# Optimization experiments

Measured on AMD Instinct MI355X. Metric: run time of the kernel, lower is better.

## Reference

```python
import jax, jax.numpy as jnp
import numpy as np

D1, D2, B, I, O = 64, 64, 32, 64, 128


def setup_inputs() -> dict:
    key = jax.random.key(0)
    ks = jax.random.split(key, 13)
    k = float(np.sqrt(1.0 / O))
    u = lambda kk, shape: jax.random.uniform(kk, shape, minval=-k, maxval=k, dtype=jnp.float32)
    return {
        "x": jax.random.normal(ks[0], (D1, D2, B, I), dtype=jnp.float32),
        "wf": u(ks[1], (2, I, O)),
        "uf": u(ks[2], (2, 2, O)),
        "biasf": u(ks[3], (2, O)),
        "wi": u(ks[4], (I, O)),
        "ui": u(ks[5], (2, O)),
        "biasi": u(ks[6], (O,)),
        "wo": u(ks[7], (I, O)),
        "uo": u(ks[8], (2, O)),
        "biaso": u(ks[9], (O,)),
        "wc": u(ks[10], (I, O)),
        "uc": u(ks[11], (2, O)),
        "biasc": u(ks[12], (O,)),
    }


def reference(x, wf, uf, biasf, wi, ui, biasi, wo, uo, biaso, wc, uc, biasc):
    # x: (D1, D2, B, I). Recurrence: cell (i,j) depends on (i-1,j) [k=0] and (i,j-1) [k=1].
    d1, d2, b, _ = x.shape
    o_dim = wi.shape[1]

    def cell(xj, s0, h0):
        # s0, h0: (2, B, O); index 0 = up-neighbor (dim 0), 1 = left-neighbor (dim 1)
        f = jax.nn.sigmoid(biasf[:, None, :]
                           + jnp.einsum('bi,lio->lbo', xj, wf)
                           + jnp.einsum('kbo,lko->lbo', h0, uf))
        i = jax.nn.sigmoid(biasi + xj @ wi + (h0 * ui[:, None, :]).sum(0))
        og = jax.nn.sigmoid(biaso + xj @ wo + (h0 * uo[:, None, :]).sum(0))
        c = jax.nn.sigmoid(biasc + xj @ wc + (h0 * uc[:, None, :]).sum(0))  # note: sigmoid, as in source
        s = i * c + (f * s0).sum(0)
        h = og * jnp.tanh(s)
        return s, h

    z_row = jnp.zeros((d2, b, o_dim), x.dtype)
    z = jnp.zeros((b, o_dim), x.dtype)

    def row_step(carry, x_row):
        s_up_row, h_up_row = carry  # (D2, B, O) each: previous row's states

        def col_step(c2, inp):
            s_left, h_left = c2
            xj, s_up, h_up = inp
            s, h = cell(xj, jnp.stack([s_up, s_left]), jnp.stack([h_up, h_left]))
            return (s, h), (s, h)

        _, (s_row, h_row) = jax.lax.scan(col_step, (z, z), (x_row, s_up_row, h_up_row))
        return (s_row, h_row), s_row

    _, s_all = jax.lax.scan(row_step, (z_row, z_row), x)
    # Original module returns reshape(s, ...) (cell state), not h -- reproduce faithfully.
    return s_all  # (D1, D2, B, O)
```

## Files before the change

kernel.cpp:

```cpp
#include <hip/hip_runtime.h>
#include <hip/hip_fp16.h>


#define P23_OFF  ((size_t)64 << 20)
#define P4_OFF   ((size_t)128 << 20)
#define GX_BYTES ((size_t)160 << 20)
#define LOG2E    1.4426950408889634f

typedef __attribute__((ext_vector_type(8))) _Float16 half8;
typedef __attribute__((ext_vector_type(2))) __fp16 fp16x2;
typedef __attribute__((ext_vector_type(4))) float f32x4;

__device__ __forceinline__ unsigned pkrtz(float a, float b) {
    union { fp16x2 h; unsigned u; } c;
    c.h = __builtin_amdgcn_cvt_pkrtz(a, b);
    return c.u;
}

__device__ __forceinline__ int diag_off(int d) {
    return (d < 64) ? ((d * (d + 1)) >> 1) : (4096 - (((127 - d) * (128 - d)) >> 1));
}

__global__ __launch_bounds__(256) void lut_kernel(int* __restrict__ lut) {
    int t = blockIdx.x * 256 + threadIdx.x;
    int i = t >> 6, j = t & 63;
    int d = i + j;
    int jmin = (d > 63) ? (d - 63) : 0;
    lut[diag_off(d) + j - jmin] = t;
}

__global__ __launch_bounds__(256) void prep_w(
    const float* __restrict__ wf, const float* __restrict__ wi,
    const float* __restrict__ wo, const float* __restrict__ wc,
    _Float16* __restrict__ wt)
{
    const int g = blockIdx.x;
    const float* W = (g == 0) ? wf : (g == 1) ? (wf + 8192)
                   : (g == 2) ? wi : (g == 3) ? wo : wc;
    const int t = threadIdx.x;
    const int o = t >> 1, k0 = (t & 1) * 32;
    _Float16 buf[32];
#pragma unroll
    for (int k = 0; k < 32; ++k)
        buf[k] = (_Float16)(-W[(k0 + k) * 128 + o] * LOG2E);
    _Float16* dst = wt + ((size_t)g * 128 + o) * 64 + k0;
#pragma unroll
    for (int q = 0; q < 4; ++q) *(half8*)(dst + q * 8) = *(half8*)(buf + q * 8);
}

__global__ __launch_bounds__(256, 2) void gemm_kernel(
    const float* __restrict__ x, const _Float16* __restrict__ wt,
    const float* __restrict__ biasf, const float* __restrict__ biasi,
    const float* __restrict__ biaso, const float* __restrict__ biasc,
    const int* __restrict__ lut, char* __restrict__ gx)
{
    __shared__ _Float16 As[128][72];
    const int t  = threadIdx.x;
    const int p0 = blockIdx.x * 128;
    const int b  = blockIdx.y;

    {
        int r = t >> 1, k0 = (t & 1) * 32;
        int cell = lut[p0 + r];
        const float* xr = x + ((size_t)cell * 32 + b) * 64 + k0;
#pragma unroll
        for (int it = 0; it < 4; ++it) {
            float4 v0 = *(const float4*)(xr + it * 8);
            float4 v1 = *(const float4*)(xr + it * 8 + 4);
            half8 h;
            h[0] = (_Float16)v0.x; h[1] = (_Float16)v0.y;
            h[2] = (_Float16)v0.z; h[3] = (_Float16)v0.w;
            h[4] = (_Float16)v1.x; h[5] = (_Float16)v1.y;
            h[6] = (_Float16)v1.z; h[7] = (_Float16)v1.w;
            *(half8*)&As[r][k0 + it * 8] = h;
        }
    }
    __syncthreads();

    const int lane = t & 63;
    const int wv   = __builtin_amdgcn_readfirstlane(t >> 6);
    const int m    = lane & 15;
    const int quad = lane >> 4;
    const int o0   = wv * 32 + m;
    const int o1   = o0 + 16;
    const size_t row0 = (size_t)(b * 128 + o0) * 4096;
    const size_t row1 = (size_t)(b * 128 + o1) * 4096;
    const int pq = p0 + quad * 4;

    auto pair_phase = [&](const _Float16* wga, const _Float16* wgb,
                          const float* bA, const float* bB, char* plane) {
        half8 ba0[2], ba1[2], bb0[2], bb1[2];
#pragma unroll
        for (int kh = 0; kh < 2; ++kh) {
            ba0[kh] = *(const half8*)(wga + o0 * 64 + kh * 32 + quad * 8);
            ba1[kh] = *(const half8*)(wga + o1 * 64 + kh * 32 + quad * 8);
            bb0[kh] = *(const half8*)(wgb + o0 * 64 + kh * 32 + quad * 8);
            bb1[kh] = *(const half8*)(wgb + o1 * 64 + kh * 32 + quad * 8);
        }
        f32x4 aA[8][2] = {}, aB[8][2] = {};
#pragma unroll
        for (int pf = 0; pf < 8; ++pf) {
            half8 af0 = *(const half8*)&As[pf * 16 + m][quad * 8];
            half8 af1 = *(const half8*)&As[pf * 16 + m][32 + quad * 8];
            aA[pf][0] = __builtin_amdgcn_mfma_f32_16x16x32_f16(af0, ba0[0], aA[pf][0], 0, 0, 0);
            aA[pf][0] = __builtin_amdgcn_mfma_f32_16x16x32_f16(af1, ba0[1], aA[pf][0], 0, 0, 0);
            aA[pf][1] = __builtin_amdgcn_mfma_f32_16x16x32_f16(af0, ba1[0], aA[pf][1], 0, 0, 0);
            aA[pf][1] = __builtin_amdgcn_mfma_f32_16x16x32_f16(af1, ba1[1], aA[pf][1], 0, 0, 0);
            aB[pf][0] = __builtin_amdgcn_mfma_f32_16x16x32_f16(af0, bb0[0], aB[pf][0], 0, 0, 0);
            aB[pf][0] = __builtin_amdgcn_mfma_f32_16x16x32_f16(af1, bb0[1], aB[pf][0], 0, 0, 0);
            aB[pf][1] = __builtin_amdgcn_mfma_f32_16x16x32_f16(af0, bb1[0], aB[pf][1], 0, 0, 0);
            aB[pf][1] = __builtin_amdgcn_mfma_f32_16x16x32_f16(af1, bb1[1], aB[pf][1], 0, 0, 0);
        }
        float sA0 = -bA[o0] * LOG2E, sA1 = -bA[o1] * LOG2E;
        float sB0 = -bB[o0] * LOG2E, sB1 = -bB[o1] * LOG2E;
#pragma unroll
        for (int pf = 0; pf < 8; ++pf) {
#pragma unroll
            for (int of = 0; of < 2; ++of) {
                float sa = of ? sA1 : sA0, sb = of ? sB1 : sB0;
                f32x4 va = aA[pf][of], vb = aB[pf][of];
                uint4 st;
                st.x = pkrtz(va[0] + sa, vb[0] + sb);
                st.y = pkrtz(va[1] + sa, vb[1] + sb);
                st.z = pkrtz(va[2] + sa, vb[2] + sb);
                st.w = pkrtz(va[3] + sa, vb[3] + sb);
                size_t row = of ? row1 : row0;
                *(uint4*)(plane + (row + pq + pf * 16) * 4) = st;
            }
        }
    };
    pair_phase(wt,            wt + 8192,     biasf, biasf + 128, gx);
    pair_phase(wt + 2 * 8192, wt + 3 * 8192, biasi, biaso,       gx + P23_OFF);

    {
        const _Float16* wg = wt + 4 * 8192;
        half8 b0[2], b1[2];
#pragma unroll
        for (int kh = 0; kh < 2; ++kh) {
            b0[kh] = *(const half8*)(wg + o0 * 64 + kh * 32 + quad * 8);
            b1[kh] = *(const half8*)(wg + o1 * 64 + kh * 32 + quad * 8);
        }
        f32x4 ac[8][2] = {};
#pragma unroll
        for (int pf = 0; pf < 8; ++pf) {
            half8 af0 = *(const half8*)&As[pf * 16 + m][quad * 8];
            half8 af1 = *(const half8*)&As[pf * 16 + m][32 + quad * 8];
            ac[pf][0] = __builtin_amdgcn_mfma_f32_16x16x32_f16(af0, b0[0], ac[pf][0], 0, 0, 0);
            ac[pf][0] = __builtin_amdgcn_mfma_f32_16x16x32_f16(af1, b0[1], ac[pf][0], 0, 0, 0);
            ac[pf][1] = __builtin_amdgcn_mfma_f32_16x16x32_f16(af0, b1[0], ac[pf][1], 0, 0, 0);
            ac[pf][1] = __builtin_amdgcn_mfma_f32_16x16x32_f16(af1, b1[1], ac[pf][1], 0, 0, 0);
        }
        float s0 = -biasc[o0] * LOG2E, s1 = -biasc[o1] * LOG2E;
        char* plane = gx + P4_OFF;
#pragma unroll
        for (int pf = 0; pf < 8; ++pf) {
#pragma unroll
            for (int of = 0; of < 2; ++of) {
                float sb = of ? s1 : s0;
                f32x4 v = ac[pf][of];
                uint2 st;
                st.x = pkrtz(v[0] + sb, v[1] + sb);
                st.y = pkrtz(v[2] + sb, v[3] + sb);
                size_t row = of ? row1 : row0;
                *(uint2*)(plane + (row + pq + pf * 16) * 2) = st;
            }
        }
    }
}

__global__ __launch_bounds__(256) void recur_kernel(
    char* __restrict__ gx,
    const float* __restrict__ uf, const float* __restrict__ ui,
    const float* __restrict__ uo, const float* __restrict__ uc)
{
    const int lane = threadIdx.x & 63;
    const int w = __builtin_amdgcn_readfirstlane(blockIdx.x * 4 + (threadIdx.x >> 6));
    const int o = w & 127;

    const float nf00 = -uf[o] * LOG2E,       nf01 = -uf[128 + o] * LOG2E;
    const float nf10 = -uf[256 + o] * LOG2E, nf11 = -uf[384 + o] * LOG2E;
    const float ni0 = -ui[o] * LOG2E, ni1 = -ui[128 + o] * LOG2E;
    const float no0 = -uo[o] * LOG2E, no1 = -uo[128 + o] * LOG2E;
    const float nc0 = -uc[o] * LOG2E, nc1 = -uc[128 + o] * LOG2E;

    const char* pc01 = gx + (size_t)w * 16384;
    const char* pc23 = gx + P23_OFF + (size_t)w * 16384;
    const char* pc4  = gx + P4_OFF + (size_t)w * 8192;
    char*       ps4  = gx + P4_OFF + (size_t)w * 8192;
    const int l4 = lane * 4, l2 = lane * 2;

    const int zm  = (lane == 0) ? 0 : -1;
    const int bpi = (lane - 1) * 4;

    float c0,c1,c2,c3,c4, n0,n1,n2,n3,n4;

#define LD3(v0_,v1_,v2_,v3_,v4_) { \
    __half2 h01 = *(const __half2*)(pc01 + l4); \
    __half2 h23 = *(const __half2*)(pc23 + l4); \
    _Float16 h4 = *(const _Float16*)(pc4 + l2); \
    v0_ = __low2float(h01); v1_ = __high2float(h01); \
    v2_ = __low2float(h23); v3_ = __high2float(h23); \
    v4_ = (float)h4; }

    LD3(c0,c1,c2,c3,c4); pc01 += 4;  pc23 += 4;  pc4 += 2;
    LD3(n0,n1,n2,n3,n4); pc01 += 8;  pc23 += 8;  pc4 += 4;

    float s_prev = 0.f, h_prev = 0.f;

    for (int d = 0; d < 127; ++d) {
        float t0,t1,t2,t3,t4;
        LD3(t0,t1,t2,t3,t4);
        int del = min(d + 3, 124 - d); del = max(del, 0);
        pc01 += del * 4; pc23 += del * 4; pc4 += del * 2;

        int slb = __builtin_amdgcn_ds_bpermute(bpi, __float_as_int(s_prev)) & zm;
        int hlb = __builtin_amdgcn_ds_bpermute(bpi, __float_as_int(h_prev)) & zm;
        float sl = __int_as_float(slb), hl = __int_as_float(hlb);

        float zf0 = fmaf(h_prev, nf00, fmaf(hl, nf01, c0));
        float zf1 = fmaf(h_prev, nf10, fmaf(hl, nf11, c1));
        float zi  = fmaf(h_prev, ni0,  fmaf(hl, ni1,  c2));
        float zo  = fmaf(h_prev, no0,  fmaf(hl, no1,  c3));
        float zc  = fmaf(h_prev, nc0,  fmaf(hl, nc1,  c4));
        float f0 = __builtin_amdgcn_rcpf(1.f + __builtin_amdgcn_exp2f(zf0));
        float f1 = __builtin_amdgcn_rcpf(1.f + __builtin_amdgcn_exp2f(zf1));
        float ig = __builtin_amdgcn_rcpf(1.f + __builtin_amdgcn_exp2f(zi));
        float og = __builtin_amdgcn_rcpf(1.f + __builtin_amdgcn_exp2f(zo));
        float cg = __builtin_amdgcn_rcpf(1.f + __builtin_amdgcn_exp2f(zc));

        float s  = fmaf(ig, cg, fmaf(f0, s_prev, f1 * sl));
        float e2 = __builtin_amdgcn_exp2f(s * (2.f * LOG2E));
        float th = fmaf(-2.f, __builtin_amdgcn_rcpf(1.f + e2), 1.f);
        float h  = og * th;

        bool act = (unsigned)(d - lane) < 64u;
        if (act) *(_Float16*)(ps4 + l2) = (_Float16)s;
        ps4 += min(d + 1, 126 - d) * 2;

        s_prev = act ? s : 0.f;
        h_prev = act ? h : 0.f;
        c0 = n0; c1 = n1; c2 = n2; c3 = n3; c4 = n4;
        n0 = t0; n1 = t1; n2 = t2; n3 = t3; n4 = t4;
    }
#undef LD3
}

__global__ __launch_bounds__(256) void transpose_kernel(
    const char* __restrict__ gx, const int* __restrict__ lut,
    float* __restrict__ out)
{
    __shared__ _Float16 T[256][80];
    const _Float16* p4 = (const _Float16*)(gx + P4_OFF);
    const int t  = threadIdx.x;
    const int p0 = blockIdx.x * 64;
    const int w0 = blockIdx.y * 256;
#pragma unroll
    for (int it = 0; it < 8; ++it) {
        int wl = it * 32 + (t >> 3), pl = (t & 7) * 8;
        *(half8*)&T[wl][pl] =
            *(const half8*)(p4 + (size_t)(w0 + wl) * 4096 + p0 + pl);
    }
    __syncthreads();
    float* ob = out + w0 + t;
#pragma unroll 4
    for (int p = 0; p < 64; ++p) {
        int cell = lut[p0 + p];
        ob[(size_t)cell * 4096] = (float)T[t][p];
    }
}

extern "C" void kernel_launch(void* const* d_in, const int* in_sizes, int n_in,
                              void* d_out, int out_size, void* d_ws, size_t ws_size,
                              hipStream_t stream) {
    const float* x     = (const float*)d_in[0];
    const float* wf    = (const float*)d_in[1];
    const float* uf    = (const float*)d_in[2];
    const float* biasf = (const float*)d_in[3];
    const float* wi    = (const float*)d_in[4];
    const float* ui    = (const float*)d_in[5];
    const float* biasi = (const float*)d_in[6];
    const float* wo    = (const float*)d_in[7];
    const float* uo    = (const float*)d_in[8];
    const float* biaso = (const float*)d_in[9];
    const float* wc    = (const float*)d_in[10];
    const float* uc    = (const float*)d_in[11];
    const float* biasc = (const float*)d_in[12];
    float* out = (float*)d_out;

    char*     gx  = (char*)d_ws;
    int*      lut = (int*)(gx + GX_BYTES);
    _Float16* wt  = (_Float16*)((char*)lut + 16384);

    lut_kernel<<<16, 256, 0, stream>>>(lut);
    prep_w<<<5, 256, 0, stream>>>(wf, wi, wo, wc, wt);
    gemm_kernel<<<dim3(32, 32), 256, 0, stream>>>(
        x, wt, biasf, biasi, biaso, biasc, lut, gx);
    recur_kernel<<<1024, 256, 0, stream>>>(gx, uf, ui, uo, uc);
    transpose_kernel<<<dim3(64, 16), 256, 0, stream>>>(gx, lut, out);
}
```

Baseline: 240.5 us.

## Pack two batch wavefronts per recurrence wave, use DPP shift, fold gate reciprocals

The recurrence kernel now runs two (batch, output) chains through one wavefront in a skewed wavefront schedule of 191 diagonal steps. This halves the grid, so fewer waves are needed and more lanes do work on each step. The left-neighbor exchange moves from ds_bpermute to a DPP row-shift, and the sigmoid gate math is merged so fewer reciprocals are needed per step. The GEMM kernel hoists its shared-memory A fragments into registers once and reuses them across all three phases. The trade-offs are more address-selection arithmetic, a longer serial loop per wave, and higher register pressure in the GEMM.

```diff
diff --git a/kernel.cpp b/kernel.cpp
--- a/kernel.cpp
+++ b/kernel.cpp
@@ -15,6 +15,10 @@
     union { fp16x2 h; unsigned u; } c;
     c.h = __builtin_amdgcn_cvt_pkrtz(a, b);
     return c.u;
+}
+__device__ __forceinline__ float wave_shr1(float v) {
+    return __int_as_float(
+        __builtin_amdgcn_update_dpp(0, __float_as_int(v), 0x138, 0xf, 0xf, true));
 }
 
 __device__ __forceinline__ int diag_off(int d) {
@@ -87,6 +91,13 @@
     const size_t row1 = (size_t)(b * 128 + o1) * 4096;
     const int pq = p0 + quad * 4;
 
+    half8 A0r[8], A1r[8];
+#pragma unroll
+    for (int pf = 0; pf < 8; ++pf) {
+        A0r[pf] = *(const half8*)&As[pf * 16 + m][quad * 8];
+        A1r[pf] = *(const half8*)&As[pf * 16 + m][32 + quad * 8];
+    }
+
     auto pair_phase = [&](const _Float16* wga, const _Float16* wgb,
                           const float* bA, const float* bB, char* plane) {
         half8 ba0[2], ba1[2], bb0[2], bb1[2];
@@ -100,16 +111,14 @@
         f32x4 aA[8][2] = {}, aB[8][2] = {};
 #pragma unroll
         for (int pf = 0; pf < 8; ++pf) {
-            half8 af0 = *(const half8*)&As[pf * 16 + m][quad * 8];
-            half8 af1 = *(const half8*)&As[pf * 16 + m][32 + quad * 8];
-            aA[pf][0] = __builtin_amdgcn_mfma_f32_16x16x32_f16(af0, ba0[0], aA[pf][0], 0, 0, 0);
-            aA[pf][0] = __builtin_amdgcn_mfma_f32_16x16x32_f16(af1, ba0[1], aA[pf][0], 0, 0, 0);
-            aA[pf][1] = __builtin_amdgcn_mfma_f32_16x16x32_f16(af0, ba1[0], aA[pf][1], 0, 0, 0);
-            aA[pf][1] = __builtin_amdgcn_mfma_f32_16x16x32_f16(af1, ba1[1], aA[pf][1], 0, 0, 0);
-            aB[pf][0] = __builtin_amdgcn_mfma_f32_16x16x32_f16(af0, bb0[0], aB[pf][0], 0, 0, 0);
-            aB[pf][0] = __builtin_amdgcn_mfma_f32_16x16x32_f16(af1, bb0[1], aB[pf][0], 0, 0, 0);
-            aB[pf][1] = __builtin_amdgcn_mfma_f32_16x16x32_f16(af0, bb1[0], aB[pf][1], 0, 0, 0);
-            aB[pf][1] = __builtin_amdgcn_mfma_f32_16x16x32_f16(af1, bb1[1], aB[pf][1], 0, 0, 0);
+            aA[pf][0] = __builtin_amdgcn_mfma_f32_16x16x32_f16(A0r[pf], ba0[0], aA[pf][0], 0, 0, 0);
+            aA[pf][0] = __builtin_amdgcn_mfma_f32_16x16x32_f16(A1r[pf], ba0[1], aA[pf][0], 0, 0, 0);
+            aA[pf][1] = __builtin_amdgcn_mfma_f32_16x16x32_f16(A0r[pf], ba1[0], aA[pf][1], 0, 0, 0);
+            aA[pf][1] = __builtin_amdgcn_mfma_f32_16x16x32_f16(A1r[pf], ba1[1], aA[pf][1], 0, 0, 0);
+            aB[pf][0] = __builtin_amdgcn_mfma_f32_16x16x32_f16(A0r[pf], bb0[0], aB[pf][0], 0, 0, 0);
+            aB[pf][0] = __builtin_amdgcn_mfma_f32_16x16x32_f16(A1r[pf], bb0[1], aB[pf][0], 0, 0, 0);
+            aB[pf][1] = __builtin_amdgcn_mfma_f32_16x16x32_f16(A0r[pf], bb1[0], aB[pf][1], 0, 0, 0);
+            aB[pf][1] = __builtin_amdgcn_mfma_f32_16x16x32_f16(A1r[pf], bb1[1], aB[pf][1], 0, 0, 0);
         }
         float sA0 = -bA[o0] * LOG2E, sA1 = -bA[o1] * LOG2E;
         float sB0 = -bB[o0] * LOG2E, sB1 = -bB[o1] * LOG2E;
@@ -143,12 +152,10 @@
         f32x4 ac[8][2] = {};
 #pragma unroll
         for (int pf = 0; pf < 8; ++pf) {
-            half8 af0 = *(const half8*)&As[pf * 16 + m][quad * 8];
-            half8 af1 = *(const half8*)&As[pf * 16 + m][32 + quad * 8];
-            ac[pf][0] = __builtin_amdgcn_mfma_f32_16x16x32_f16(af0, b0[0], ac[pf][0], 0, 0, 0);
-            ac[pf][0] = __builtin_amdgcn_mfma_f32_16x16x32_f16(af1, b0[1], ac[pf][0], 0, 0, 0);
-            ac[pf][1] = __builtin_amdgcn_mfma_f32_16x16x32_f16(af0, b1[0], ac[pf][1], 0, 0, 0);
-            ac[pf][1] = __builtin_amdgcn_mfma_f32_16x16x32_f16(af1, b1[1], ac[pf][1], 0, 0, 0);
+            ac[pf][0] = __builtin_amdgcn_mfma_f32_16x16x32_f16(A0r[pf], b0[0], ac[pf][0], 0, 0, 0);
+            ac[pf][0] = __builtin_amdgcn_mfma_f32_16x16x32_f16(A1r[pf], b0[1], ac[pf][0], 0, 0, 0);
+            ac[pf][1] = __builtin_amdgcn_mfma_f32_16x16x32_f16(A0r[pf], b1[0], ac[pf][1], 0, 0, 0);
+            ac[pf][1] = __builtin_amdgcn_mfma_f32_16x16x32_f16(A1r[pf], b1[1], ac[pf][1], 0, 0, 0);
         }
         float s0 = -biasc[o0] * LOG2E, s1 = -biasc[o1] * LOG2E;
         char* plane = gx + P4_OFF;
@@ -183,66 +190,89 @@
     const float no0 = -uo[o] * LOG2E, no1 = -uo[128 + o] * LOG2E;
     const float nc0 = -uc[o] * LOG2E, nc1 = -uc[128 + o] * LOG2E;
 
-    const char* pc01 = gx + (size_t)w * 16384;
-    const char* pc23 = gx + P23_OFF + (size_t)w * 16384;
-    const char* pc4  = gx + P4_OFF + (size_t)w * 8192;
-    char*       ps4  = gx + P4_OFF + (size_t)w * 8192;
+    const char* b01 = gx + (size_t)w * 16384;
+    const char* b23 = gx + P23_OFF + (size_t)w * 16384;
+    const char* b4  = gx + P4_OFF + (size_t)w * 8192;
+    char*       s4  = gx + P4_OFF + (size_t)w * 8192;
     const int l4 = lane * 4, l2 = lane * 2;
 
-    const int zm  = (lane == 0) ? 0 : -1;
-    const int bpi = (lane - 1) * 4;
-
+    int QA01 = 0, QA4 = 0;
+    int QB01 = 1 << 25, QB4 = 1 << 24;
+    int TA4 = 0, TB4 = 1 << 24;
+
+    int iv = -lane;
     float c0,c1,c2,c3,c4, n0,n1,n2,n3,n4;
 
-#define LD3(v0_,v1_,v2_,v3_,v4_) { \
-    __half2 h01 = *(const __half2*)(pc01 + l4); \
-    __half2 h23 = *(const __half2*)(pc23 + l4); \
-    _Float16 h4 = *(const _Float16*)(pc4 + l2); \
+#define LDSEL(v0_,v1_,v2_,v3_,v4_, PF) { \
+    bool inApf_ = (unsigned)(iv + (PF)) < 64u; \
+    int s01_ = (inApf_ ? QA01 : QB01) + l4; \
+    int s4_  = (inApf_ ? QA4  : QB4)  + l2; \
+    __half2 h01 = *(const __half2*)(b01 + s01_); \
+    __half2 h23 = *(const __half2*)(b23 + s01_); \
+    _Float16 h4 = *(const _Float16*)(b4 + s4_); \
     v0_ = __low2float(h01); v1_ = __high2float(h01); \
     v2_ = __low2float(h23); v3_ = __high2float(h23); \
     v4_ = (float)h4; }
 
-    LD3(c0,c1,c2,c3,c4); pc01 += 4;  pc23 += 4;  pc4 += 2;
-    LD3(n0,n1,n2,n3,n4); pc01 += 8;  pc23 += 8;  pc4 += 4;
+    LDSEL(c0,c1,c2,c3,c4, 0);  QA01 += 1 * 4;  QA4 += 1 * 2;
+    LDSEL(n0,n1,n2,n3,n4, 1);  QA01 += 2 * 4;  QA4 += 2 * 2;
 
     float s_prev = 0.f, h_prev = 0.f;
 
-    for (int d = 0; d < 127; ++d) {
+#pragma unroll 2
+    for (int d = 0; d < 191; ++d) {
         float t0,t1,t2,t3,t4;
-        LD3(t0,t1,t2,t3,t4);
-        int del = min(d + 3, 124 - d); del = max(del, 0);
-        pc01 += del * 4; pc23 += del * 4; pc4 += del * 2;
-
-        int slb = __builtin_amdgcn_ds_bpermute(bpi, __float_as_int(s_prev)) & zm;
-        int hlb = __builtin_amdgcn_ds_bpermute(bpi, __float_as_int(h_prev)) & zm;
-        float sl = __int_as_float(slb), hl = __int_as_float(hlb);
-
-        float zf0 = fmaf(h_prev, nf00, fmaf(hl, nf01, c0));
-        float zf1 = fmaf(h_prev, nf10, fmaf(hl, nf11, c1));
-        float zi  = fmaf(h_prev, ni0,  fmaf(hl, ni1,  c2));
-        float zo  = fmaf(h_prev, no0,  fmaf(hl, no1,  c3));
-        float zc  = fmaf(h_prev, nc0,  fmaf(hl, nc1,  c4));
-        float f0 = __builtin_amdgcn_rcpf(1.f + __builtin_amdgcn_exp2f(zf0));
-        float f1 = __builtin_amdgcn_rcpf(1.f + __builtin_amdgcn_exp2f(zf1));
-        float ig = __builtin_amdgcn_rcpf(1.f + __builtin_amdgcn_exp2f(zi));
-        float og = __builtin_amdgcn_rcpf(1.f + __builtin_amdgcn_exp2f(zo));
-        float cg = __builtin_amdgcn_rcpf(1.f + __builtin_amdgcn_exp2f(zc));
-
-        float s  = fmaf(ig, cg, fmaf(f0, s_prev, f1 * sl));
-        float e2 = __builtin_amdgcn_exp2f(s * (2.f * LOG2E));
-        float th = fmaf(-2.f, __builtin_amdgcn_rcpf(1.f + e2), 1.f);
+        LDSEL(t0,t1,t2,t3,t4, 2);
+        {
+            int adA = min(d + 3, 124 - d); adA = max(adA, 0);
+            int adB = min(d - 61, 188 - d); adB = max(adB, 0);
+            QA01 += adA * 4; QA4 += adA * 2;
+            QB01 += adB * 4; QB4 += adB * 2;
+        }
+
+        float sl = wave_shr1(s_prev);
+        float hl = wave_shr1(h_prev);
+        bool rs = (iv & 63) == 0;
+        float su = rs ? 0.f : s_prev;
+        float hu = rs ? 0.f : h_prev;
+
+        float zf0 = fmaf(hu, nf00, fmaf(hl, nf01, c0));
+        float zf1 = fmaf(hu, nf10, fmaf(hl, nf11, c1));
+        float zi  = fmaf(hu, ni0,  fmaf(hl, ni1,  c2));
+        float zo  = fmaf(hu, no0,  fmaf(hl, no1,  c3));
+        float zc  = fmaf(hu, nc0,  fmaf(hl, nc1,  c4));
+
+        float E0 = __builtin_amdgcn_exp2f(zf0);
+        float E1 = __builtin_amdgcn_exp2f(zf1);
+        float Ei = __builtin_amdgcn_exp2f(zi);
+        float Eo = __builtin_amdgcn_exp2f(zo);
+        float Ec = __builtin_amdgcn_exp2f(zc);
+        float A0 = 1.f + E0, A1 = 1.f + E1;
+        float F   = fmaf(su, A1, sl * A0) * __builtin_amdgcn_rcpf(A0 * A1);
+        float icg = __builtin_amdgcn_rcpf(fmaf(Ei, Ec, (Ei + Ec) + 1.f));
+        float og  = __builtin_amdgcn_rcpf(1.f + Eo);
+
+        float s  = icg + F;
+        float E2 = __builtin_amdgcn_exp2f((s + s) * LOG2E);
+        float th = fmaf(-2.f, __builtin_amdgcn_rcpf(E2 + 1.f), 1.f);
         float h  = og * th;
 
-        bool act = (unsigned)(d - lane) < 64u;
-        if (act) *(_Float16*)(ps4 + l2) = (_Float16)s;
-        ps4 += min(d + 1, 126 - d) * 2;
-
-        s_prev = act ? s : 0.f;
-        h_prev = act ? h : 0.f;
+        bool act = (unsigned)iv < 128u;
+        bool inA = (unsigned)iv < 64u;
+        int selS = (inA ? TA4 : TB4) + l2;
+        if (act) *(_Float16*)(s4 + selS) = (_Float16)s;
+        {
+            int aA = min(d + 1, 126 - d); aA = max(aA, 0);
+            int aB = min(d - 63, 190 - d); aB = max(aB, 0);
+            TA4 += aA * 2; TB4 += aB * 2;
+        }
+
+        s_prev = s; h_prev = h;
+        iv += 1;
         c0 = n0; c1 = n1; c2 = n2; c3 = n3; c4 = n4;
         n0 = t0; n1 = t1; n2 = t2; n3 = t3; n4 = t4;
     }
-#undef LD3
+#undef LDSEL
 }
 
 __global__ __launch_bounds__(256) void transpose_kernel(
@@ -295,6 +325,6 @@
     prep_w<<<5, 256, 0, stream>>>(wf, wi, wo, wc, wt);
     gemm_kernel<<<dim3(32, 32), 256, 0, stream>>>(
         x, wt, biasf, biasi, biaso, biasc, lut, gx);
-    recur_kernel<<<1024, 256, 0, stream>>>(gx, uf, ui, uo, uc);
+    recur_kernel<<<512, 256, 0, stream>>>(gx, uf, ui, uo, uc);
     transpose_kernel<<<dim3(64, 16), 256, 0, stream>>>(gx, lut, out);
 }
```

Result: slower. 257.2 us (+6.9%).

## Use DPP lane shift, merge sigmoid reciprocals, and coalesce GEMM input loads

Applied to the files above, without the earlier changes.

The recurrence kernel now shifts the left-neighbour state with a DPP row-shift instead of two ds_bpermute LDS round trips. It also merges the forget-gate and input/candidate sigmoid reciprocals algebraically, which cuts the number of rcp instructions on the serial critical path. The GEMM kernel's input staging now uses 16 threads per row with float4 loads over 8 rows instead of 2 threads per row with 32 floats each, which should improve coalescing. One risk is that DPP row_shr with bound_ctrl only shifts within 16-lane rows, so lanes 16, 32 and 48 get zero instead of their neighbour, which may be a correctness bug.

```diff
diff --git a/kernel.cpp b/kernel.cpp
--- a/kernel.cpp
+++ b/kernel.cpp
@@ -8,6 +8,7 @@
 #define LOG2E    1.4426950408889634f
 
 typedef __attribute__((ext_vector_type(8))) _Float16 half8;
+typedef __attribute__((ext_vector_type(4))) _Float16 half4;
 typedef __attribute__((ext_vector_type(2))) __fp16 fp16x2;
 typedef __attribute__((ext_vector_type(4))) float f32x4;
 
@@ -15,6 +16,10 @@
     union { fp16x2 h; unsigned u; } c;
     c.h = __builtin_amdgcn_cvt_pkrtz(a, b);
     return c.u;
+}
+__device__ __forceinline__ float wave_shr1(float v) {
+    return __int_as_float(
+        __builtin_amdgcn_update_dpp(0, __float_as_int(v), 0x138, 0xf, 0xf, true));
 }
 
 __device__ __forceinline__ int diag_off(int d) {
@@ -60,19 +65,17 @@
     const int b  = blockIdx.y;
 
     {
-        int r = t >> 1, k0 = (t & 1) * 32;
-        int cell = lut[p0 + r];
-        const float* xr = x + ((size_t)cell * 32 + b) * 64 + k0;
-#pragma unroll
-        for (int it = 0; it < 4; ++it) {
-            float4 v0 = *(const float4*)(xr + it * 8);
-            float4 v1 = *(const float4*)(xr + it * 8 + 4);
-            half8 h;
-            h[0] = (_Float16)v0.x; h[1] = (_Float16)v0.y;
-            h[2] = (_Float16)v0.z; h[3] = (_Float16)v0.w;
-            h[4] = (_Float16)v1.x; h[5] = (_Float16)v1.y;
-            h[6] = (_Float16)v1.z; h[7] = (_Float16)v1.w;
-            *(half8*)&As[r][k0 + it * 8] = h;
+        int r0 = t >> 4;
+        int c4 = (t & 15) * 4;
+#pragma unroll
+        for (int it = 0; it < 8; ++it) {
+            int r = r0 + it * 16;
+            int cell = lut[p0 + r];
+            float4 v = *(const float4*)(x + ((size_t)cell * 32 + b) * 64 + c4);
+            half4 h;
+            h[0] = (_Float16)v.x; h[1] = (_Float16)v.y;
+            h[2] = (_Float16)v.z; h[3] = (_Float16)v.w;
+            *(half4*)&As[r][c4] = h;
         }
     }
     __syncthreads();
@@ -189,9 +192,6 @@
     char*       ps4  = gx + P4_OFF + (size_t)w * 8192;
     const int l4 = lane * 4, l2 = lane * 2;
 
-    const int zm  = (lane == 0) ? 0 : -1;
-    const int bpi = (lane - 1) * 4;
-
     float c0,c1,c2,c3,c4, n0,n1,n2,n3,n4;
 
 #define LD3(v0_,v1_,v2_,v3_,v4_) { \
@@ -213,24 +213,28 @@
         int del = min(d + 3, 124 - d); del = max(del, 0);
         pc01 += del * 4; pc23 += del * 4; pc4 += del * 2;
 
-        int slb = __builtin_amdgcn_ds_bpermute(bpi, __float_as_int(s_prev)) & zm;
-        int hlb = __builtin_amdgcn_ds_bpermute(bpi, __float_as_int(h_prev)) & zm;
-        float sl = __int_as_float(slb), hl = __int_as_float(hlb);
+        float sl = wave_shr1(s_prev);
+        float hl = wave_shr1(h_prev);
 
         float zf0 = fmaf(h_prev, nf00, fmaf(hl, nf01, c0));
         float zf1 = fmaf(h_prev, nf10, fmaf(hl, nf11, c1));
         float zi  = fmaf(h_prev, ni0,  fmaf(hl, ni1,  c2));
         float zo  = fmaf(h_prev, no0,  fmaf(hl, no1,  c3));
         float zc  = fmaf(h_prev, nc0,  fmaf(hl, nc1,  c4));
-        float f0 = __builtin_amdgcn_rcpf(1.f + __builtin_amdgcn_exp2f(zf0));
-        float f1 = __builtin_amdgcn_rcpf(1.f + __builtin_amdgcn_exp2f(zf1));
-        float ig = __builtin_amdgcn_rcpf(1.f + __builtin_amdgcn_exp2f(zi));
-        float og = __builtin_amdgcn_rcpf(1.f + __builtin_amdgcn_exp2f(zo));
-        float cg = __builtin_amdgcn_rcpf(1.f + __builtin_amdgcn_exp2f(zc));
-
-        float s  = fmaf(ig, cg, fmaf(f0, s_prev, f1 * sl));
-        float e2 = __builtin_amdgcn_exp2f(s * (2.f * LOG2E));
-        float th = fmaf(-2.f, __builtin_amdgcn_rcpf(1.f + e2), 1.f);
+
+        float E0 = __builtin_amdgcn_exp2f(zf0);
+        float E1 = __builtin_amdgcn_exp2f(zf1);
+        float Ei = __builtin_amdgcn_exp2f(zi);
+        float Eo = __builtin_amdgcn_exp2f(zo);
+        float Ec = __builtin_amdgcn_exp2f(zc);
+        float A0 = 1.f + E0, A1 = 1.f + E1;
+        float F   = fmaf(s_prev, A1, sl * A0) * __builtin_amdgcn_rcpf(A0 * A1);
+        float icg = __builtin_amdgcn_rcpf(fmaf(Ei, Ec, (Ei + Ec) + 1.f));
+        float og  = __builtin_amdgcn_rcpf(1.f + Eo);
+
+        float s  = icg + F;
+        float E2 = __builtin_amdgcn_exp2f((s + s) * LOG2E);
+        float th = fmaf(-2.f, __builtin_amdgcn_rcpf(E2 + 1.f), 1.f);
         float h  = og * th;
 
         bool act = (unsigned)(d - lane) < 64u;
```

After: 250.8 us. +4.3%, slower.
